# Performance work log

Hardware: AMD Instinct MI355X
Metric: run time of the kernel (lower is better)

## Reference

```python
import jax, jax.numpy as jnp
import numpy as np
import math

B, N, C, H, DC = 1, 320, 128, 4, 32  # batch, residues, pair channels, heads, per-head dim


def setup_inputs() -> dict:
    key = jax.random.key(0)
    ks = jax.random.split(key, 8)
    s = lambda k, shape: jax.random.normal(k, shape, dtype=jnp.float32) * 0.02
    return {
        "x2d": jax.random.normal(ks[0], (B, N, N, C), dtype=jnp.float32),
        "mask": jnp.ones((B, N, N), dtype=jnp.float32),
        "ln_g": jnp.ones((C,), jnp.float32),
        "ln_b": jnp.zeros((C,), jnp.float32),
        "wq": s(ks[1], (C, H * DC)),
        "wk": s(ks[2], (C, H * DC)),
        "wv": s(ks[3], (C, H * DC)),
        "wb": s(ks[4], (C, H)),
        "wg": s(ks[5], (C, H * DC)),
        "bg": jnp.zeros((H * DC,), jnp.float32),
        "wo": s(ks[6], (H * DC, C)),
        "bo": jnp.zeros((C,), jnp.float32),
    }


def reference(x2d, mask, ln_g, ln_b, wq, wk, wv, wb, wg, bg, wo, bo):
    # ending_node = False -> no transpose
    # LayerNorm (torch uses biased variance, eps=1e-5)
    mu = x2d.mean(-1, keepdims=True)
    var = ((x2d - mu) ** 2).mean(-1, keepdims=True)
    xn = (x2d - mu) * jax.lax.rsqrt(var + 1e-5) * ln_g + ln_b  # [B,N,N,C]

    sh = xn.shape[:-1]  # (B, N, N)
    q = (xn @ wq).reshape(*sh, H, DC)
    k = (xn @ wk).reshape(*sh, H, DC)
    v = (xn @ wv).reshape(*sh, H, DC)

    scale = 1.0 / math.sqrt(DC)
    aff = jnp.einsum('bmihc,bmjhc->bmhij', q * scale, k)  # [B,N,H,N,N]

    # pair bias: [B,I,J,H] -> [B,1,H,I,J], broadcast over the row axis m
    bterm = jnp.einsum('bijc,ch->bhij', xn, wb)[:, None]
    mask_bias = (100000.0 * (mask - 1.0))[:, :, None, None, :]  # [B,N,1,1,N]

    weights = jax.nn.softmax(aff + bterm + mask_bias, axis=-1)

    g = jax.nn.sigmoid((xn @ wg + bg).reshape(*sh, H, DC))
    out = jnp.einsum('bmhqk,bmkhc->bmqhc', weights, v) * g  # [B,N,N,H,DC]
    out = out.reshape(*sh, H * DC) @ wo + bo  # [B,N,N,C]
    return out
```

## Files before the change

kernel.cpp:

```cpp
#include <hip/hip_runtime.h>
#include <hip/hip_bf16.h>

typedef __attribute__((ext_vector_type(8))) short bf16x8;
typedef __attribute__((ext_vector_type(4))) float f32x4;
typedef __attribute__((ext_vector_type(4))) unsigned short u16x4;

#define DEVI static __device__ __forceinline__

DEVI float bf2f(unsigned short u) {
    union { unsigned int ui; float f; } c; c.ui = ((unsigned int)u) << 16; return c.f;
}
DEVI unsigned short f2bf(float f) {
    union { float f; unsigned int ui; } c; c.f = f;
    unsigned int u = c.ui;
    u += 0x7FFFu + ((u >> 16) & 1u);
    return (unsigned short)(u >> 16);
}
DEVI unsigned int pk2bf(float a, float b) {
    union { __hip_bfloat162 h; unsigned int u; } c;
    c.h = __float22bfloat162_rn(make_float2(a, b));
    return c.u;
}

#define NRES 320
#define NN   102400
#define CCH  128
#define NPAD 328
#define PPAD 40

#define LOG2E 1.4426950408889634f
#define QSCALE (0.17677669529663687f * 1.4426950408889634f)

__global__ __launch_bounds__(256) void k_ln_bias(
    const float* __restrict__ x2d, const float* __restrict__ ln_g,
    const float* __restrict__ ln_b, const float* __restrict__ wb,
    unsigned short* __restrict__ xn, float* __restrict__ bterm)
{
    int wave = threadIdx.x >> 6, lane = threadIdx.x & 63;
    int r = blockIdx.x * 4 + wave;
    int c0 = lane * 2;
    float2 x = *(const float2*)(x2d + (size_t)r * CCH + c0);
    float s = x.x + x.y, sq = x.x * x.x + x.y * x.y;
    #pragma unroll
    for (int m = 1; m < 64; m <<= 1) { s += __shfl_xor(s, m, 64); sq += __shfl_xor(sq, m, 64); }
    float mu = s * (1.0f / 128.0f);
    float var = sq * (1.0f / 128.0f) - mu * mu;
    float rstd = rsqrtf(var + 1e-5f);
    float xn0 = (x.x - mu) * rstd * ln_g[c0] + ln_b[c0];
    float xn1 = (x.y - mu) * rstd * ln_g[c0 + 1] + ln_b[c0 + 1];
    *(unsigned int*)(xn + (size_t)r * CCH + c0) = pk2bf(xn0, xn1);
    float4 w0 = *(const float4*)(wb + c0 * 4);
    float4 w1 = *(const float4*)(wb + c0 * 4 + 4);
    float b0 = xn0 * w0.x + xn1 * w1.x;
    float b1 = xn0 * w0.y + xn1 * w1.y;
    float b2 = xn0 * w0.z + xn1 * w1.z;
    float b3 = xn0 * w0.w + xn1 * w1.w;
    #pragma unroll
    for (int m = 1; m < 64; m <<= 1) {
        b0 += __shfl_xor(b0, m, 64); b1 += __shfl_xor(b1, m, 64);
        b2 += __shfl_xor(b2, m, 64); b3 += __shfl_xor(b3, m, 64);
    }
    if (lane == 0) {
        bterm[0 * NN + r] = b0 * LOG2E; bterm[1 * NN + r] = b1 * LOG2E;
        bterm[2 * NN + r] = b2 * LOG2E; bterm[3 * NN + r] = b3 * LOG2E;
    }
}

__global__ __launch_bounds__(256) void k_proj(
    const unsigned short* __restrict__ xn,
    const float* __restrict__ wq, const float* __restrict__ wk,
    const float* __restrict__ wv, const float* __restrict__ wg,
    const float* __restrict__ bg,
    unsigned short* __restrict__ qkvg)
{
    __shared__ unsigned short A[128][136];
    __shared__ unsigned short Bt[128][136];
    int m0 = blockIdx.x * 128;
    int nt = blockIdx.y;
    int t = threadIdx.x;
    const float* wsrc = (nt == 0) ? wq : (nt == 1) ? wk : (nt == 2) ? wv : wg;
    #pragma unroll
    for (int it = 0; it < 8; ++it) {
        int idx = it * 256 + t;
        int row = idx >> 4, chunk = idx & 15;
        *(bf16x8*)(&A[row][chunk * 8]) = *(const bf16x8*)(xn + (size_t)(m0 + row) * CCH + chunk * 8);
    }
    {
        int n = t & 127, p = t >> 7;
        const float* col = wsrc + n;
        #pragma unroll
        for (int q = 0; q < 8; ++q) {
            int k0 = p * 64 + q * 8;
            union { unsigned int u[4]; bf16x8 v; } pk;
            #pragma unroll
            for (int z = 0; z < 4; ++z)
                pk.u[z] = pk2bf(col[(size_t)(k0 + 2 * z) * 128], col[(size_t)(k0 + 2 * z + 1) * 128]);
            *(bf16x8*)(&Bt[n][k0]) = pk.v;
        }
    }
    __syncthreads();
    int wave = t >> 6, lane = t & 63;
    int wr = (wave >> 1) * 64, wc = (wave & 1) * 64;
    int li = lane & 15, lk = (lane >> 4) * 8;
    f32x4 acc[4][4] = {};
    #pragma unroll
    for (int kk = 0; kk < 4; ++kk) {
        bf16x8 af[4], bfr[4];
        #pragma unroll
        for (int i = 0; i < 4; ++i) af[i] = *(const bf16x8*)(&A[wr + i * 16 + li][kk * 32 + lk]);
        #pragma unroll
        for (int j = 0; j < 4; ++j) bfr[j] = *(const bf16x8*)(&Bt[wc + j * 16 + li][kk * 32 + lk]);
        __builtin_amdgcn_s_setprio(1);
        #pragma unroll
        for (int i = 0; i < 4; ++i)
            #pragma unroll
            for (int j = 0; j < 4; ++j)
                acc[i][j] = __builtin_amdgcn_mfma_f32_16x16x32_bf16(af[i], bfr[j], acc[i][j], 0, 0, 0);
        __builtin_amdgcn_s_setprio(0);
    }
    int rbase = (lane >> 4) * 4;
    bool isg = (nt == 3), isq = (nt == 0);
    #pragma unroll
    for (int i = 0; i < 4; ++i) {
        #pragma unroll
        for (int j = 0; j < 4; ++j) {
            int col = wc + j * 16 + li;
            int gcol = nt * 128 + col;
            #pragma unroll
            for (int r = 0; r < 4; ++r) {
                int grow = m0 + wr + i * 16 + rbase + r;
                float v = acc[i][j][r];
                if (isg) { v += bg[col]; v = 1.0f / (1.0f + __expf(-v)); }
                if (isq) v *= QSCALE;
                qkvg[(size_t)grow * 512 + gcol] = f2bf(v);
            }
        }
    }
}

__global__ __launch_bounds__(256) void k_attn(
    const unsigned short* __restrict__ qkvg,
    const float* __restrict__ bterm,
    const float* __restrict__ mask,
    unsigned short* __restrict__ opre)
{
    __shared__ unsigned short Kl[320][40];
    __shared__ unsigned short VT[32][NPAD];
    __shared__ unsigned short Pl[4][16][PPAD];
    __shared__ float mb[320];
    int bid = blockIdx.x;
    int m = bid >> 2, h = bid & 3;
    int t = threadIdx.x;
    size_t base = (size_t)m * NRES * 512;
    for (int j = t; j < NRES; j += 256) {
        const bf16x8* src = (const bf16x8*)(qkvg + base + (size_t)j * 512 + 128 + h * 32);
        bf16x8* dst = (bf16x8*)(&Kl[j][0]);
        dst[0] = src[0]; dst[1] = src[1]; dst[2] = src[2]; dst[3] = src[3];
    }
    {
        int dc = t & 31, jg = t >> 5;
        #pragma unroll 8
        for (int jj = 0; jj < 40; jj += 2) {
            int j = jg * 40 + jj;
            unsigned short v0 = qkvg[base + (size_t)j * 512 + 256 + h * 32 + dc];
            unsigned short v1 = qkvg[base + (size_t)(j + 1) * 512 + 256 + h * 32 + dc];
            *(unsigned int*)(&VT[dc][j]) = (unsigned int)v0 | ((unsigned int)v1 << 16);
        }
    }
    for (int j = t; j < NRES; j += 256) mb[j] = (100000.0f * LOG2E) * (mask[(size_t)m * NRES + j] - 1.0f);
    __syncthreads();

    int wave = t >> 6, lane = t & 63;
    int li = lane & 15, lg = lane >> 4;
    for (int c = 0; c < 5; ++c) {
        int i0 = wave * 80 + c * 16;
        int i = i0 + li;
        size_t qrow = base + (size_t)i * 512;
        bf16x8 qf = *(const bf16x8*)(qkvg + qrow + h * 32 + lg * 8);
        const float* brow = bterm + (size_t)h * NN + (size_t)i * NRES;
        f32x4 z = {0.f, 0.f, 0.f, 0.f};
        float mrun = -3.0e38f, sum = 0.0f;
        f32x4 o0 = {0.f, 0.f, 0.f, 0.f}, o1 = {0.f, 0.f, 0.f, 0.f};
        #pragma unroll 1
        for (int ph = 0; ph < 5; ++ph) {
            f32x4 st[4];
            __builtin_amdgcn_s_setprio(1);
            #pragma unroll
            for (int jf = 0; jf < 4; ++jf) {
                bf16x8 kf = *(const bf16x8*)(&Kl[ph * 64 + jf * 16 + li][lg * 8]);
                st[jf] = __builtin_amdgcn_mfma_f32_16x16x32_bf16(kf, qf, z, 0, 0, 0);
            }
            __builtin_amdgcn_s_setprio(0);
            float mx = mrun;
            #pragma unroll
            for (int jf = 0; jf < 4; ++jf) {
                int j0 = ph * 64 + jf * 16 + lg * 4;
                float4 bb = *(const float4*)(brow + j0);
                float4 mm = *(const float4*)(&mb[j0]);
                st[jf][0] += bb.x + mm.x;
                st[jf][1] += bb.y + mm.y;
                st[jf][2] += bb.z + mm.z;
                st[jf][3] += bb.w + mm.w;
                mx = fmaxf(mx, fmaxf(fmaxf(st[jf][0], st[jf][1]), fmaxf(st[jf][2], st[jf][3])));
            }
            mx = fmaxf(mx, __shfl_xor(mx, 16, 64));
            mx = fmaxf(mx, __shfl_xor(mx, 32, 64));
            if (ph) {
                float corr = __builtin_amdgcn_exp2f(mrun - mx);
                sum *= corr;
                #pragma unroll
                for (int r = 0; r < 4; ++r) { o0[r] *= corr; o1[r] *= corr; }
            }
            mrun = mx;
            #pragma unroll
            for (int half = 0; half < 2; ++half) {
                #pragma unroll
                for (int jf2 = 0; jf2 < 2; ++jf2) {
                    int jf = half * 2 + jf2;
                    float p0 = __builtin_amdgcn_exp2f(st[jf][0] - mx);
                    float p1 = __builtin_amdgcn_exp2f(st[jf][1] - mx);
                    float p2 = __builtin_amdgcn_exp2f(st[jf][2] - mx);
                    float p3 = __builtin_amdgcn_exp2f(st[jf][3] - mx);
                    sum += (p0 + p1) + (p2 + p3);
                    unsigned int* dst = (unsigned int*)(&Pl[wave][li][jf2 * 16 + lg * 4]);
                    dst[0] = pk2bf(p0, p1); dst[1] = pk2bf(p2, p3);
                }
                __builtin_amdgcn_s_setprio(1);
                {
                    bf16x8 pf = *(const bf16x8*)(&Pl[wave][li][lg * 8]);
                    bf16x8 va = *(const bf16x8*)(&VT[li][ph * 64 + half * 32 + lg * 8]);
                    bf16x8 vb = *(const bf16x8*)(&VT[16 + li][ph * 64 + half * 32 + lg * 8]);
                    o0 = __builtin_amdgcn_mfma_f32_16x16x32_bf16(va, pf, o0, 0, 0, 0);
                    o1 = __builtin_amdgcn_mfma_f32_16x16x32_bf16(vb, pf, o1, 0, 0, 0);
                }
                __builtin_amdgcn_s_setprio(0);
            }
        }
        sum += __shfl_xor(sum, 16, 64);
        sum += __shfl_xor(sum, 32, 64);
        float inv = 1.0f / sum;
        size_t orow = ((size_t)m * NRES + i) * CCH + h * 32;
        #pragma unroll
        for (int df = 0; df < 2; ++df) {
            f32x4 o = df ? o1 : o0;
            int dcb = df * 16 + lg * 4;
            u16x4 gv = *(const u16x4*)(qkvg + qrow + 384 + h * 32 + dcb);
            u16x4 ov;
            #pragma unroll
            for (int r = 0; r < 4; ++r) ov[r] = f2bf(o[r] * inv * bf2f(gv[r]));
            *(u16x4*)(opre + orow + dcb) = ov;
        }
    }
}

__global__ __launch_bounds__(256) void k_out(
    const unsigned short* __restrict__ opre, const float* __restrict__ wo,
    const float* __restrict__ bo, float* __restrict__ out)
{
    __shared__ unsigned short A[128][136];
    __shared__ unsigned short Bt[128][136];
    int m0 = blockIdx.x * 128;
    int t = threadIdx.x;
    #pragma unroll
    for (int it = 0; it < 8; ++it) {
        int idx = it * 256 + t;
        int row = idx >> 4, chunk = idx & 15;
        *(bf16x8*)(&A[row][chunk * 8]) = *(const bf16x8*)(opre + (size_t)(m0 + row) * CCH + chunk * 8);
    }
    {
        int n = t & 127, p = t >> 7;
        const float* col = wo + n;
        #pragma unroll
        for (int q = 0; q < 8; ++q) {
            int k0 = p * 64 + q * 8;
            union { unsigned int u[4]; bf16x8 v; } pk;
            #pragma unroll
            for (int z = 0; z < 4; ++z)
                pk.u[z] = pk2bf(col[(size_t)(k0 + 2 * z) * 128], col[(size_t)(k0 + 2 * z + 1) * 128]);
            *(bf16x8*)(&Bt[n][k0]) = pk.v;
        }
    }
    __syncthreads();
    int wave = t >> 6, lane = t & 63;
    int wr = (wave >> 1) * 64, wc = (wave & 1) * 64;
    int li = lane & 15, lk = (lane >> 4) * 8;
    f32x4 acc[4][4] = {};
    #pragma unroll
    for (int kk = 0; kk < 4; ++kk) {
        bf16x8 af[4], bfr[4];
        #pragma unroll
        for (int i = 0; i < 4; ++i) af[i] = *(const bf16x8*)(&A[wr + i * 16 + li][kk * 32 + lk]);
        #pragma unroll
        for (int j = 0; j < 4; ++j) bfr[j] = *(const bf16x8*)(&Bt[wc + j * 16 + li][kk * 32 + lk]);
        __builtin_amdgcn_s_setprio(1);
        #pragma unroll
        for (int i = 0; i < 4; ++i)
            #pragma unroll
            for (int j = 0; j < 4; ++j)
                acc[i][j] = __builtin_amdgcn_mfma_f32_16x16x32_bf16(af[i], bfr[j], acc[i][j], 0, 0, 0);
        __builtin_amdgcn_s_setprio(0);
    }
    int rbase = (lane >> 4) * 4;
    #pragma unroll
    for (int i = 0; i < 4; ++i) {
        #pragma unroll
        for (int j = 0; j < 4; ++j) {
            int col = wc + j * 16 + li;
            #pragma unroll
            for (int r = 0; r < 4; ++r) {
                int grow = m0 + wr + i * 16 + rbase + r;
                out[(size_t)grow * CCH + col] = acc[i][j][r] + bo[col];
            }
        }
    }
}

extern "C" void kernel_launch(void* const* d_in, const int* in_sizes, int n_in,
                              void* d_out, int out_size, void* d_ws, size_t ws_size,
                              hipStream_t stream) {
    const float* x2d  = (const float*)d_in[0];
    const float* mask = (const float*)d_in[1];
    const float* ln_g = (const float*)d_in[2];
    const float* ln_b = (const float*)d_in[3];
    const float* wq   = (const float*)d_in[4];
    const float* wk   = (const float*)d_in[5];
    const float* wv   = (const float*)d_in[6];
    const float* wb   = (const float*)d_in[7];
    const float* wg   = (const float*)d_in[8];
    const float* bg   = (const float*)d_in[9];
    const float* wo   = (const float*)d_in[10];
    const float* bo   = (const float*)d_in[11];
    float* out = (float*)d_out;

    char* ws = (char*)d_ws;
    unsigned short* xn    = (unsigned short*)ws;
    unsigned short* qkvg  = (unsigned short*)(ws + 26214400);
    float*          bterm = (float*)(ws + 26214400 + 104857600);
    unsigned short* opre  = xn;

    if (ws_size < (size_t)(26214400 + 104857600 + 1638400)) return;

    k_ln_bias<<<25600, 256, 0, stream>>>(x2d, ln_g, ln_b, wb, xn, bterm);
    k_proj<<<dim3(800, 4), 256, 0, stream>>>(xn, wq, wk, wv, wg, bg, qkvg);
    k_attn<<<1280, 256, 0, stream>>>(qkvg, bterm, mask, opre);
    k_out<<<800, 256, 0, stream>>>(opre, wo, bo, out);
}
```

Baseline: 213.6 us.

## Shuffle softmax probabilities in registers and prefetch pair bias in attention kernel

The attention kernel drops the per-wave shared-memory staging buffer for softmax probabilities. The P fragment for the PV MFMA is now built with cross-lane shuffles, which removes LDS writes and reads from the inner loop. Pair-bias rows are prefetched one phase ahead into registers so global load latency overlaps the QK MFMAs and softmax. The K tile load is spread over more threads, and the s_setprio hints are removed. The cost is higher register pressure and extra shuffle instructions in place of LDS traffic.

```diff
diff --git a/kernel.cpp b/kernel.cpp
--- a/kernel.cpp
+++ b/kernel.cpp
@@ -26,7 +26,6 @@
 #define NN   102400
 #define CCH  128
 #define NPAD 328
-#define PPAD 40
 
 #define LOG2E 1.4426950408889634f
 #define QSCALE (0.17677669529663687f * 1.4426950408889634f)
@@ -146,16 +145,15 @@
 {
     __shared__ unsigned short Kl[320][40];
     __shared__ unsigned short VT[32][NPAD];
-    __shared__ unsigned short Pl[4][16][PPAD];
     __shared__ float mb[320];
     int bid = blockIdx.x;
     int m = bid >> 2, h = bid & 3;
     int t = threadIdx.x;
     size_t base = (size_t)m * NRES * 512;
-    for (int j = t; j < NRES; j += 256) {
-        const bf16x8* src = (const bf16x8*)(qkvg + base + (size_t)j * 512 + 128 + h * 32);
-        bf16x8* dst = (bf16x8*)(&Kl[j][0]);
-        dst[0] = src[0]; dst[1] = src[1]; dst[2] = src[2]; dst[3] = src[3];
+    for (int idx = t; idx < NRES * 4; idx += 256) {
+        int row = idx >> 2, q = idx & 3;
+        *(bf16x8*)(&Kl[row][q * 8]) =
+            *(const bf16x8*)(qkvg + base + (size_t)row * 512 + 128 + h * 32 + q * 8);
     }
     {
         int dc = t & 31, jg = t >> 5;
@@ -172,31 +170,43 @@
 
     int wave = t >> 6, lane = t & 63;
     int li = lane & 15, lg = lane >> 4;
+    int selhi = lg >> 1;
+    int srcA = li + ((lane & 16) << 1);
+    int srcB = srcA + 16;
     for (int c = 0; c < 5; ++c) {
-        int i0 = wave * 80 + c * 16;
-        int i = i0 + li;
+        int i = wave * 80 + c * 16 + li;
         size_t qrow = base + (size_t)i * 512;
         bf16x8 qf = *(const bf16x8*)(qkvg + qrow + h * 32 + lg * 8);
         const float* brow = bterm + (size_t)h * NN + (size_t)i * NRES;
         f32x4 z = {0.f, 0.f, 0.f, 0.f};
         float mrun = -3.0e38f, sum = 0.0f;
-        f32x4 o0 = {0.f, 0.f, 0.f, 0.f}, o1 = {0.f, 0.f, 0.f, 0.f};
+        f32x4 o0 = z, o1 = z;
+        float4 bb0 = *(const float4*)(brow + lg * 4);
+        float4 bb1 = *(const float4*)(brow + 16 + lg * 4);
+        float4 bb2 = *(const float4*)(brow + 32 + lg * 4);
+        float4 bb3 = *(const float4*)(brow + 48 + lg * 4);
         #pragma unroll 1
         for (int ph = 0; ph < 5; ++ph) {
             f32x4 st[4];
-            __builtin_amdgcn_s_setprio(1);
             #pragma unroll
             for (int jf = 0; jf < 4; ++jf) {
                 bf16x8 kf = *(const bf16x8*)(&Kl[ph * 64 + jf * 16 + li][lg * 8]);
                 st[jf] = __builtin_amdgcn_mfma_f32_16x16x32_bf16(kf, qf, z, 0, 0, 0);
             }
-            __builtin_amdgcn_s_setprio(0);
+            float4 bn0, bn1, bn2, bn3;
+            if (ph < 4) {
+                const float* bnx = brow + (ph + 1) * 64 + lg * 4;
+                bn0 = *(const float4*)(bnx);
+                bn1 = *(const float4*)(bnx + 16);
+                bn2 = *(const float4*)(bnx + 32);
+                bn3 = *(const float4*)(bnx + 48);
+            }
             float mx = mrun;
             #pragma unroll
             for (int jf = 0; jf < 4; ++jf) {
                 int j0 = ph * 64 + jf * 16 + lg * 4;
-                float4 bb = *(const float4*)(brow + j0);
                 float4 mm = *(const float4*)(&mb[j0]);
+                float4 bb = (jf == 0) ? bb0 : (jf == 1) ? bb1 : (jf == 2) ? bb2 : bb3;
                 st[jf][0] += bb.x + mm.x;
                 st[jf][1] += bb.y + mm.y;
                 st[jf][2] += bb.z + mm.z;
@@ -213,28 +223,34 @@
             }
             mrun = mx;
             #pragma unroll
-            for (int half = 0; half < 2; ++half) {
-                #pragma unroll
-                for (int jf2 = 0; jf2 < 2; ++jf2) {
-                    int jf = half * 2 + jf2;
-                    float p0 = __builtin_amdgcn_exp2f(st[jf][0] - mx);
-                    float p1 = __builtin_amdgcn_exp2f(st[jf][1] - mx);
-                    float p2 = __builtin_amdgcn_exp2f(st[jf][2] - mx);
-                    float p3 = __builtin_amdgcn_exp2f(st[jf][3] - mx);
-                    sum += (p0 + p1) + (p2 + p3);
-                    unsigned int* dst = (unsigned int*)(&Pl[wave][li][jf2 * 16 + lg * 4]);
-                    dst[0] = pk2bf(p0, p1); dst[1] = pk2bf(p2, p3);
-                }
-                __builtin_amdgcn_s_setprio(1);
-                {
-                    bf16x8 pf = *(const bf16x8*)(&Pl[wave][li][lg * 8]);
-                    bf16x8 va = *(const bf16x8*)(&VT[li][ph * 64 + half * 32 + lg * 8]);
-                    bf16x8 vb = *(const bf16x8*)(&VT[16 + li][ph * 64 + half * 32 + lg * 8]);
-                    o0 = __builtin_amdgcn_mfma_f32_16x16x32_bf16(va, pf, o0, 0, 0, 0);
-                    o1 = __builtin_amdgcn_mfma_f32_16x16x32_bf16(vb, pf, o1, 0, 0, 0);
-                }
-                __builtin_amdgcn_s_setprio(0);
-            }
+            for (int w = 0; w < 2; ++w) {
+                int jfA = w * 2, jfB = w * 2 + 1;
+                float e0 = __builtin_amdgcn_exp2f(st[jfA][0] - mx);
+                float e1 = __builtin_amdgcn_exp2f(st[jfA][1] - mx);
+                float e2 = __builtin_amdgcn_exp2f(st[jfA][2] - mx);
+                float e3 = __builtin_amdgcn_exp2f(st[jfA][3] - mx);
+                float f0 = __builtin_amdgcn_exp2f(st[jfB][0] - mx);
+                float f1 = __builtin_amdgcn_exp2f(st[jfB][1] - mx);
+                float f2 = __builtin_amdgcn_exp2f(st[jfB][2] - mx);
+                float f3 = __builtin_amdgcn_exp2f(st[jfB][3] - mx);
+                sum += ((e0 + e1) + (e2 + e3)) + ((f0 + f1) + (f2 + f3));
+                unsigned int q0 = pk2bf(e0, e1), q1 = pk2bf(e2, e3);
+                unsigned int q2 = pk2bf(f0, f1), q3 = pk2bf(f2, f3);
+                unsigned int t0 = __shfl((int)q0, srcA, 64), t2 = __shfl((int)q2, srcA, 64);
+                unsigned int t1 = __shfl((int)q1, srcA, 64), t3 = __shfl((int)q3, srcA, 64);
+                unsigned int u0 = __shfl((int)q0, srcB, 64), u2 = __shfl((int)q2, srcB, 64);
+                unsigned int u1 = __shfl((int)q1, srcB, 64), u3 = __shfl((int)q3, srcB, 64);
+                union { unsigned int u[4]; bf16x8 v; } pf;
+                pf.u[0] = selhi ? t2 : t0;
+                pf.u[1] = selhi ? t3 : t1;
+                pf.u[2] = selhi ? u2 : u0;
+                pf.u[3] = selhi ? u3 : u1;
+                bf16x8 va = *(const bf16x8*)(&VT[li][ph * 64 + w * 32 + lg * 8]);
+                bf16x8 vb = *(const bf16x8*)(&VT[16 + li][ph * 64 + w * 32 + lg * 8]);
+                o0 = __builtin_amdgcn_mfma_f32_16x16x32_bf16(va, pf.v, o0, 0, 0, 0);
+                o1 = __builtin_amdgcn_mfma_f32_16x16x32_bf16(vb, pf.v, o1, 0, 0, 0);
+            }
+            bb0 = bn0; bb1 = bn1; bb2 = bn2; bb3 = bn3;
         }
         sum += __shfl_xor(sum, 16, 64);
         sum += __shfl_xor(sum, 32, 64);
```

Result: no change. 211.7 us (-0.9%).
